# Kernel optimization log

Measured on AMD Instinct MI355X. Metric: run time of the kernel, lower is better.

The kernel has to match this reference:

```python
import jax, jax.numpy as jnp
import numpy as np

B, D, I = 16384, 2048, 2048


def setup_inputs() -> dict:
    key = jax.random.key(0)
    kx, kh, kw = jax.random.split(key, 3)
    x = jax.random.normal(kx, (B, I), dtype=jnp.float32)
    h = jax.random.normal(kh, (B, D), dtype=jnp.float32)
    # input projection weight (Linear, no bias): [d_model, inpt_size]
    W_ih = jax.random.normal(kw, (D, I), dtype=jnp.float32) * 0.02
    # orthogonal-ish hidden transition (torch uses an SVD-orthogonal block),
    # well-conditioned so the inverse is exact and stable
    rng = np.random.default_rng(0)
    q, _ = np.linalg.qr(rng.standard_normal((D, D)).astype(np.float64))
    W_hh = jnp.asarray(q, dtype=jnp.float32)
    W_inv = jnp.asarray(np.linalg.inv(q), dtype=jnp.float32)  # buffer self.inv
    return {"x": x, "h": h, "W_ih": W_ih, "W_hh": W_hh, "W_inv": W_inv}


def reference(x, h, W_ih, W_hh, W_inv):
    # outs = inpt_linear(x) : [B, D]
    outs = jnp.einsum("bi,di->bd", x, W_ih)
    not_trig = outs[..., -1] >= -1.0          # [B]
    h_last = h[..., -1]                        # [B]
    m_fwd = ((h_last > 0) & not_trig)[..., None]   # forward rotation branch
    m_inv = ((h_last < 0) & not_trig)[..., None]   # inverse rotation branch
    m_pass = (~not_trig)[..., None]                # passthrough branch
    hW = h @ W_hh   # torch.matmul(h, weight_hh) (no transpose)
    hI = h @ W_inv  # torch.matmul(h, inv)
    zero = jnp.zeros((), dtype=outs.dtype)
    return (outs
            + jnp.where(m_fwd, hW, zero)
            + jnp.where(m_inv, hI, zero)
            + jnp.where(m_pass, h, zero))
```

## Files before the change

kernel.cpp:

```cpp
#include <hip/hip_runtime.h>
#include <hip/hip_bf16.h>
#include <stdint.h>

#define B_ROWS 16384
#define DIM 2048
#define BK 64
#define NT 96

typedef float f32x4 __attribute__((ext_vector_type(4)));
typedef short bf16x8 __attribute__((ext_vector_type(8)));
using u16 = unsigned short;
using u32 = unsigned int;

__device__ __forceinline__ u32 pack_bf2(float a, float b) {
  __hip_bfloat162 t = __float22bfloat162_rn(float2{a, b});
  union { __hip_bfloat162 b2; u32 u; } cv;
  cv.b2 = t;
  return cv.u;
}

__device__ __forceinline__ u16 f2bf_rne(float f) {
  union { float f; u32 u; } v;
  v.f = f;
  u32 u = v.u;
  u32 r = u + 0x7FFFu + ((u >> 16) & 1u);
  return (u16)(r >> 16);
}

__device__ __forceinline__ void gload16(const void* g, void* l) {
  __builtin_amdgcn_global_load_lds(
      (const __attribute__((address_space(1))) u32*)g,
      (__attribute__((address_space(3))) u32*)l, 16, 0, 0);
}

__global__ __launch_bounds__(256) void k_prep(
    const float* __restrict__ x, const float* __restrict__ h,
    const float* __restrict__ W_ih, int* __restrict__ flags,
    u16* __restrict__ xb, u16* __restrict__ hF, u16* __restrict__ hI) {
  int row = blockIdx.x * 4 + (threadIdx.x >> 6);
  int lane = threadIdx.x & 63;
  const float* xr = x + (size_t)row * DIM;
  const float* hr = h + (size_t)row * DIM;
  const float* wr = W_ih + (size_t)(DIM - 1) * DIM;
  u16* xbr = xb + (size_t)row * DIM;
  double s = 0.0;
  u32 hp[16];
#pragma unroll
  for (int i = 0; i < 8; ++i) {
    int idx = (i * 64 + lane) * 4;
    f32x4 xv = *(const f32x4*)(xr + idx);
    f32x4 wv = *(const f32x4*)(wr + idx);
    f32x4 hv = *(const f32x4*)(hr + idx);
    s += (double)xv.x * wv.x + (double)xv.y * wv.y +
         (double)xv.z * wv.z + (double)xv.w * wv.w;
    *(uint2*)(xbr + idx) = uint2{pack_bf2(xv.x, xv.y), pack_bf2(xv.z, xv.w)};
    hp[2 * i] = pack_bf2(hv.x, hv.y);
    hp[2 * i + 1] = pack_bf2(hv.z, hv.w);
  }
#pragma unroll
  for (int off = 32; off > 0; off >>= 1) s += __shfl_xor(s, off);
  float hl = hr[DIM - 1];
  int f = (s < -1.0) ? 2 : (hl > 0.f ? 0 : (hl < 0.f ? 1 : 3));
  if (lane == 0) flags[row] = f;
  uint2 z{0u, 0u};
  u16* hFr = hF + (size_t)row * DIM;
  u16* hIr = hI + (size_t)row * DIM;
#pragma unroll
  for (int i = 0; i < 8; ++i) {
    int idx = (i * 64 + lane) * 4;
    uint2 p{hp[2 * i], hp[2 * i + 1]};
    *(uint2*)(hFr + idx) = (f == 0) ? p : z;
    *(uint2*)(hIr + idx) = (f == 1) ? p : z;
  }
}

__global__ __launch_bounds__(256) void k_flags_fb(
    const float* __restrict__ x, const float* __restrict__ h,
    const float* __restrict__ W_ih, int* __restrict__ flags) {
  int row = blockIdx.x * 4 + (threadIdx.x >> 6);
  int lane = threadIdx.x & 63;
  const float* xr = x + (size_t)row * DIM;
  const float* wr = W_ih + (size_t)(DIM - 1) * DIM;
  double s = 0.0;
#pragma unroll
  for (int i = 0; i < 8; ++i) {
    int idx = (i * 64 + lane) * 4;
    f32x4 xv = *(const f32x4*)(xr + idx);
    f32x4 wv = *(const f32x4*)(wr + idx);
    s += (double)xv.x * wv.x + (double)xv.y * wv.y +
         (double)xv.z * wv.z + (double)xv.w * wv.w;
  }
#pragma unroll
  for (int off = 32; off > 0; off >>= 1) s += __shfl_xor(s, off);
  if (lane == 0) {
    float hl = h[(size_t)row * DIM + (DIM - 1)];
    flags[row] = (s < -1.0) ? 2 : (hl > 0.f ? 0 : (hl < 0.f ? 1 : 3));
  }
}

__global__ __launch_bounds__(256) void k_convert(const float* __restrict__ src,
                                                 u16* __restrict__ dst) {
  size_t i = ((size_t)blockIdx.x * 256 + threadIdx.x) * 4;
  f32x4 v = *(const f32x4*)(src + i);
  *(uint2*)(dst + i) = uint2{pack_bf2(v.x, v.y), pack_bf2(v.z, v.w)};
}

__global__ __launch_bounds__(256) void k_transpose(const float* __restrict__ src,
                                                   u16* __restrict__ dst) {
  __shared__ float tile[32][33];
  int k0 = blockIdx.x * 32;
  int n0 = blockIdx.y * 32;
  int tx = threadIdx.x & 31;
  int ty = threadIdx.x >> 5;
#pragma unroll
  for (int i = 0; i < 4; ++i)
    tile[ty + 8 * i][tx] = src[(size_t)(k0 + ty + 8 * i) * DIM + n0 + tx];
  __syncthreads();
#pragma unroll
  for (int i = 0; i < 4; ++i)
    dst[(size_t)(n0 + ty + 8 * i) * DIM + k0 + tx] = f2bf_rne(tile[tx][ty + 8 * i]);
}

__global__ __launch_bounds__(512, 2) void k_gemm8(
    const u16* __restrict__ xb, const u16* __restrict__ hF,
    const u16* __restrict__ hI, const u16* __restrict__ Wih,
    const u16* __restrict__ WhhT, const u16* __restrict__ WinvT,
    const int* __restrict__ flags, const float* __restrict__ h,
    float* __restrict__ out) {
  __shared__ __attribute__((aligned(128))) char smem[131072];

  int o = blockIdx.x;
  int swz = (o & 7) * 64 + (o >> 3);
  int brow = (swz >> 3) * 256;
  int bcol = (swz & 7) * 256;

  int t = threadIdx.x;
  int lane = t & 63;
  int wave = t >> 6;
  int wr = wave >> 2;
  int wc = wave & 3;

  int sx16 = (((lane & 3) ^ ((lane >> 3) & 3)) << 4);
  int fA = (((lane >> 4) ^ ((lane >> 1) & 3)) << 4);
  int arowbase = wr * 128 + (lane & 15);
  int browbase = wc * 64 + (lane & 15);

  auto stage = [&](int T, int isB, int kk) {
    if (T >= NT) T -= NT;
    int seg = T >> 5;
    int kt = T & 31;
    const u16* mat = isB ? (seg == 0 ? Wih : seg == 1 ? WhhT : WinvT)
                         : (seg == 0 ? xb : seg == 1 ? hF : hI);
    int r0 = isB ? bcol : brow;
    size_t gb = (size_t)(r0 + wave * 32 + (lane >> 2)) * (DIM * 2) +
                (size_t)kt * 128 + (size_t)kk * 64 + (size_t)sx16;
    char* ldst = smem + ((T & 1) << 16) + kk * 32768 + isB * 16384 +
                 (wave * 32) * 64;
    gload16((const char*)mat + gb, ldst);
    gload16((const char*)mat + gb + (size_t)16 * (DIM * 2), ldst + 1024);
  };

  f32x4 acc[8][4] = {};
  bf16x8 aF[4], bF[4];

  stage(0, 0, 0); stage(0, 1, 0); stage(0, 0, 1);
  stage(0, 1, 1); stage(1, 0, 0); stage(1, 1, 0);
  asm volatile("s_waitcnt vmcnt(8)" ::: "memory");
  __builtin_amdgcn_s_barrier();

#define PHASE(KK, MH, RDB, STT, STB, STKK, DOVM)                               \
  {                                                                            \
    const char* Ab_ = smem + buf + (KK) * 32768;                               \
    _Pragma("unroll") for (int m = 0; m < 4; ++m)                              \
        aF[m] = *(const bf16x8*)(Ab_ +                                         \
                                 (arowbase + (MH) * 64 + m * 16) * 64 + fA);   \
    if (RDB) {                                                                 \
      _Pragma("unroll") for (int n = 0; n < 4; ++n)                            \
          bF[n] = *(const bf16x8*)(Ab_ + 16384 +                               \
                                   (browbase + n * 16) * 64 + fA);             \
    }                                                                          \
    stage(STT, STB, STKK);                                                     \
    __builtin_amdgcn_s_barrier();                                              \
    asm volatile("s_waitcnt lgkmcnt(0)" ::: "memory");                         \
    __builtin_amdgcn_sched_barrier(0);                                         \
    __builtin_amdgcn_s_setprio(1);                                             \
    _Pragma("unroll") for (int m = 0; m < 4; ++m)                              \
        _Pragma("unroll") for (int n = 0; n < 4; ++n)                          \
            acc[(MH) * 4 + m][n] = __builtin_amdgcn_mfma_f32_16x16x32_bf16(    \
                aF[m], bF[n], acc[(MH) * 4 + m][n], 0, 0, 0);                  \
    __builtin_amdgcn_s_setprio(0);                                             \
    if (DOVM) asm volatile("s_waitcnt vmcnt(8)" ::: "memory");                 \
    __builtin_amdgcn_s_barrier();                                              \
  }

#pragma unroll 1
  for (int T = 0; T < NT; ++T) {
    const int buf = (T & 1) << 16;
    PHASE(0, 0, 1, T + 1, 0, 1, 0)
    PHASE(0, 1, 0, T + 1, 1, 1, 1)
    PHASE(1, 0, 1, T + 2, 0, 0, 0)
    PHASE(1, 1, 0, T + 2, 1, 0, 1)
  }
#undef PHASE
  asm volatile("s_waitcnt vmcnt(0)" ::: "memory");

#pragma unroll
  for (int mi = 0; mi < 8; ++mi) {
    int rbase = brow + wr * 128 + (mi >> 2) * 64 + (mi & 3) * 16 + (lane >> 4) * 4;
#pragma unroll
    for (int j = 0; j < 4; ++j) {
      int row = rbase + j;
      bool pass = (flags[row] == 2);
#pragma unroll
      for (int n = 0; n < 4; ++n) {
        int col = bcol + wc * 64 + n * 16 + (lane & 15);
        float v = acc[mi][n][j];
        if (pass) v += h[(size_t)row * DIM + col];
        out[(size_t)row * DIM + col] = v;
      }
    }
  }
}

#define BM 128
#define BN 128
__global__ __launch_bounds__(256, 2) void k_gemm_fb(
    const float* __restrict__ x, const float* __restrict__ h,
    const u16* __restrict__ Wih, const u16* __restrict__ WhhT,
    const u16* __restrict__ WinvT, const int* __restrict__ flags,
    float* __restrict__ out) {
  __shared__ char smem[(BM + BN) * BK * 2];
  char* sA = smem;
  char* sB = smem + BM * BK * 2;

  int o = blockIdx.x;
  int swz = (o & 7) * ((int)gridDim.x >> 3) + (o >> 3);
  int brow = (swz >> 4) * BM;
  int bcol = (swz & 15) * BN;

  int t = threadIdx.x;
  int lane = t & 63;
  int wave = t >> 6;
  int wrow = (wave >> 1) * 64;
  int wcol = (wave & 1) * 64;

  f32x4 acc[4][4] = {};
  int sc = t & 15;
  int sr0 = t >> 4;

  int aOff[4][2], bOff[4][2];
#pragma unroll
  for (int m = 0; m < 4; ++m)
#pragma unroll
    for (int kk = 0; kk < 2; ++kk) {
      int ar = wrow + m * 16 + (lane & 15);
      aOff[m][kk] = ar * (BK * 2) + ((kk * 64 + (lane >> 4) * 16) ^ ((ar & 7) << 4));
      int br = wcol + m * 16 + (lane & 15);
      bOff[m][kk] = br * (BK * 2) + ((kk * 64 + (lane >> 4) * 16) ^ ((br & 7) << 4));
    }

#pragma unroll 1
  for (int seg = 0; seg < 3; ++seg) {
    const float* Asrc = (seg == 0) ? x : h;
    const u16* Bsrc = (seg == 0) ? Wih : (seg == 1) ? WhhT : WinvT;
    int want = seg - 1;

    float rmask[8];
#pragma unroll
    for (int i = 0; i < 8; ++i) {
      int r = sr0 + 16 * i;
      rmask[i] = (want < 0 || flags[brow + r] == want) ? 1.f : 0.f;
    }

#pragma unroll 1
    for (int k0 = 0; k0 < DIM; k0 += BK) {
      __syncthreads();
#pragma unroll
      for (int i = 0; i < 8; ++i) {
        int r = sr0 + 16 * i;
        f32x4 v = *(const f32x4*)(Asrc + (size_t)(brow + r) * DIM + k0 + sc * 4);
        float msk = rmask[i];
        int off = r * (BK * 2) + ((sc * 8) ^ ((r & 7) << 4));
        *(uint2*)(sA + off) =
            uint2{pack_bf2(v.x * msk, v.y * msk), pack_bf2(v.z * msk, v.w * msk)};
      }
#pragma unroll
      for (int i = 0; i < 4; ++i) {
        int ch = t + 256 * i;
        int r = ch >> 3;
        int c = ch & 7;
        uint4 v = *(const uint4*)(Bsrc + (size_t)(bcol + r) * DIM + k0 + c * 8);
        int off = r * (BK * 2) + ((c * 16) ^ ((r & 7) << 4));
        *(uint4*)(sB + off) = v;
      }
      __syncthreads();
      bf16x8 aF2[4][2], bF2[4][2];
#pragma unroll
      for (int m = 0; m < 4; ++m)
#pragma unroll
        for (int kk = 0; kk < 2; ++kk) {
          aF2[m][kk] = *(const bf16x8*)(sA + aOff[m][kk]);
          bF2[m][kk] = *(const bf16x8*)(sB + bOff[m][kk]);
        }
#pragma unroll
      for (int kk = 0; kk < 2; ++kk)
#pragma unroll
        for (int m = 0; m < 4; ++m)
#pragma unroll
          for (int n = 0; n < 4; ++n)
            acc[m][n] = __builtin_amdgcn_mfma_f32_16x16x32_bf16(
                aF2[m][kk], bF2[n][kk], acc[m][n], 0, 0, 0);
    }
  }

#pragma unroll
  for (int m = 0; m < 4; ++m) {
    int rbase = brow + wrow + m * 16 + (lane >> 4) * 4;
#pragma unroll
    for (int j = 0; j < 4; ++j) {
      int row = rbase + j;
      bool pass = (flags[row] == 2);
#pragma unroll
      for (int n = 0; n < 4; ++n) {
        int col = bcol + wcol + n * 16 + (lane & 15);
        float v = acc[m][n][j];
        if (pass) v += h[(size_t)row * DIM + col];
        out[(size_t)row * DIM + col] = v;
      }
    }
  }
}

extern "C" void kernel_launch(void* const* d_in, const int* in_sizes, int n_in,
                              void* d_out, int out_size, void* d_ws, size_t ws_size,
                              hipStream_t stream) {
  const float* x = (const float*)d_in[0];
  const float* h = (const float*)d_in[1];
  const float* W_ih = (const float*)d_in[2];
  const float* W_hh = (const float*)d_in[3];
  const float* W_inv = (const float*)d_in[4];
  float* out = (float*)d_out;

  char* ws = (char*)d_ws;
  int* flags = (int*)ws;
  u16* WihB = (u16*)(ws + (64 << 10));
  u16* WhhT = WihB + (size_t)DIM * DIM;
  u16* WinvT = WhhT + (size_t)DIM * DIM;
  u16* xb = WinvT + (size_t)DIM * DIM;
  u16* hF = xb + (size_t)B_ROWS * DIM;
  u16* hI = hF + (size_t)B_ROWS * DIM;
  size_t need = (size_t)(64 << 10) + 3ull * DIM * DIM * 2 + 3ull * B_ROWS * DIM * 2;

  k_convert<<<(DIM * DIM / 4) / 256, 256, 0, stream>>>(W_ih, WihB);
  k_transpose<<<dim3(DIM / 32, DIM / 32), 256, 0, stream>>>(W_hh, WhhT);
  k_transpose<<<dim3(DIM / 32, DIM / 32), 256, 0, stream>>>(W_inv, WinvT);

  if (ws_size >= need) {
    k_prep<<<B_ROWS / 4, 256, 0, stream>>>(x, h, W_ih, flags, xb, hF, hI);
    k_gemm8<<<(B_ROWS / 256) * (DIM / 256), 512, 0, stream>>>(
        xb, hF, hI, WihB, WhhT, WinvT, flags, h, out);
  } else {
    k_flags_fb<<<B_ROWS / 4, 256, 0, stream>>>(x, h, W_ih, flags);
    k_gemm_fb<<<(B_ROWS / BM) * (DIM / BN), 256, 0, stream>>>(x, h, WihB, WhhT,
                                                              WinvT, flags, out);
  }
}
```

Before: 506.5 us.

## Merge four half-tile phases into two full-tile phases per K step

Each loop iteration now runs two phases instead of four. Each phase loads all eight A fragments and four B fragments, issues both global-to-LDS stages together, and runs 32 MFMAs under a single barrier. The aim is to halve the barrier and wait count per iteration and give the scheduler longer MFMA runs between syncs. The cost is more VGPRs for the A fragments and fewer barriers guarding LDS reuse. That leaves a possible race on the K-half region being refilled while slower waves may still be reading it.

```diff
diff --git a/kernel.cpp b/kernel.cpp
--- a/kernel.cpp
+++ b/kernel.cpp
@@ -161,45 +161,43 @@
   };
 
   f32x4 acc[8][4] = {};
-  bf16x8 aF[4], bF[4];
-
-  stage(0, 0, 0); stage(0, 1, 0); stage(0, 0, 1);
-  stage(0, 1, 1); stage(1, 0, 0); stage(1, 1, 0);
+  bf16x8 aF[8], bF[4];
+
+  stage(0, 0, 0); stage(0, 1, 0);
+  stage(0, 0, 1); stage(0, 1, 1);
+  stage(1, 0, 0); stage(1, 1, 0);
   asm volatile("s_waitcnt vmcnt(8)" ::: "memory");
   __builtin_amdgcn_s_barrier();
 
-#define PHASE(KK, MH, RDB, STT, STB, STKK, DOVM)                               \
+#define PHASE(KK, STT, STKK)                                                   \
   {                                                                            \
     const char* Ab_ = smem + buf + (KK) * 32768;                               \
-    _Pragma("unroll") for (int m = 0; m < 4; ++m)                              \
-        aF[m] = *(const bf16x8*)(Ab_ +                                         \
-                                 (arowbase + (MH) * 64 + m * 16) * 64 + fA);   \
-    if (RDB) {                                                                 \
-      _Pragma("unroll") for (int n = 0; n < 4; ++n)                            \
-          bF[n] = *(const bf16x8*)(Ab_ + 16384 +                               \
-                                   (browbase + n * 16) * 64 + fA);             \
+    _Pragma("unroll") for (int m = 0; m < 4; ++m) {                            \
+      aF[m] = *(const bf16x8*)(Ab_ + (arowbase + m * 16) * 64 + fA);           \
+      aF[4 + m] = *(const bf16x8*)(Ab_ + (arowbase + 64 + m * 16) * 64 + fA);  \
     }                                                                          \
-    stage(STT, STB, STKK);                                                     \
+    _Pragma("unroll") for (int n = 0; n < 4; ++n)                              \
+        bF[n] = *(const bf16x8*)(Ab_ + 16384 + (browbase + n * 16) * 64 + fA); \
+    stage(STT, 0, STKK);                                                       \
+    stage(STT, 1, STKK);                                                       \
+    asm volatile("s_waitcnt vmcnt(8)" ::: "memory");                           \
     __builtin_amdgcn_s_barrier();                                              \
     asm volatile("s_waitcnt lgkmcnt(0)" ::: "memory");                         \
     __builtin_amdgcn_sched_barrier(0);                                         \
     __builtin_amdgcn_s_setprio(1);                                             \
-    _Pragma("unroll") for (int m = 0; m < 4; ++m)                              \
-        _Pragma("unroll") for (int n = 0; n < 4; ++n)                          \
-            acc[(MH) * 4 + m][n] = __builtin_amdgcn_mfma_f32_16x16x32_bf16(    \
-                aF[m], bF[n], acc[(MH) * 4 + m][n], 0, 0, 0);                  \
+    _Pragma("unroll") for (int mh = 0; mh < 2; ++mh)                           \
+        _Pragma("unroll") for (int m = 0; m < 4; ++m)                          \
+            _Pragma("unroll") for (int n = 0; n < 4; ++n)                      \
+                acc[mh * 4 + m][n] = __builtin_amdgcn_mfma_f32_16x16x32_bf16(  \
+                    aF[mh * 4 + m], bF[n], acc[mh * 4 + m][n], 0, 0, 0);       \
     __builtin_amdgcn_s_setprio(0);                                             \
-    if (DOVM) asm volatile("s_waitcnt vmcnt(8)" ::: "memory");                 \
-    __builtin_amdgcn_s_barrier();                                              \
   }
 
 #pragma unroll 1
   for (int T = 0; T < NT; ++T) {
     const int buf = (T & 1) << 16;
-    PHASE(0, 0, 1, T + 1, 0, 1, 0)
-    PHASE(0, 1, 0, T + 1, 1, 1, 1)
-    PHASE(1, 0, 1, T + 2, 0, 0, 0)
-    PHASE(1, 1, 0, T + 2, 1, 0, 1)
+    PHASE(0, T + 1, 1)
+    PHASE(1, T + 2, 0)
   }
 #undef PHASE
   asm volatile("s_waitcnt vmcnt(0)" ::: "memory");
```

Measured after the change: 503.2 us. About the same (-0.6%).
